# Kernel optimization log

Measured on AMD Instinct MI355X. Metric: run time of the kernel, lower is better.

## Reference

```python
import jax, jax.numpy as jnp
import numpy as np

N = 100000      # nodes
M_HE = 200000   # hyperedges
E = 2000000     # incidences (edge_index columns)
IN, HID, OUT, NT = 16, 64, 64, 2


def setup_inputs() -> dict:
    key = jax.random.key(0)
    ks = jax.random.split(key, 16)
    s = 0.05
    return {
        "x": jax.random.normal(ks[0], (N, IN), jnp.float32),
        "h_prev": jax.random.normal(ks[1], (N, HID), jnp.float32),
        "edge_nodes": jax.random.randint(ks[2], (E,), 0, N, dtype=jnp.int32),
        "edge_hedges": jax.random.randint(ks[3], (E,), 0, M_HE, dtype=jnp.int32),
        "edge_attr": jax.random.randint(ks[4], (E,), 0, NT, dtype=jnp.int32),
        "W_conv": jax.random.normal(ks[5], (NT, IN, HID), jnp.float32) * s,
        "b_conv": jax.random.normal(ks[6], (NT, HID), jnp.float32) * s,
        "W_mix": jax.random.normal(ks[7], (NT * HID, HID), jnp.float32) * s,
        "b_mix": jax.random.normal(ks[8], (HID,), jnp.float32) * s,
        "W_ih": jax.random.normal(ks[9], (3 * HID, HID), jnp.float32) * s,
        "W_hh": jax.random.normal(ks[10], (3 * HID, HID), jnp.float32) * s,
        "b_ih": jax.random.normal(ks[11], (3 * HID,), jnp.float32) * s,
        "b_hh": jax.random.normal(ks[12], (3 * HID,), jnp.float32) * s,
        "W_out": jax.random.normal(ks[13], (HID, OUT), jnp.float32) * s,
        "b_out": jax.random.normal(ks[14], (OUT,), jnp.float32) * s,
    }


def _hconv(x, W, b, nodes, hedges, mask_f):
    """PyG HypergraphConv: out = D^-1 H B^-1 H^T (x W) + b, restricted to
    incidences where mask_f==1 (replaces torch nonzero()-based slicing)."""
    xw = x @ W                                                   # [N, HID]
    Bdeg = jax.ops.segment_sum(mask_f, hedges, num_segments=M_HE)  # |e| per hyperedge
    Ddeg = jax.ops.segment_sum(mask_f, nodes, num_segments=N)      # deg per node
    Binv = jnp.where(Bdeg > 0, 1.0 / Bdeg, 0.0)
    Dinv = jnp.where(Ddeg > 0, 1.0 / Ddeg, 0.0)
    # node -> hyperedge gather/scatter
    e_feat = jax.ops.segment_sum(xw[nodes] * mask_f[:, None], hedges,
                                 num_segments=M_HE) * Binv[:, None]  # [M_HE, HID]
    # hyperedge -> node gather/scatter
    out = jax.ops.segment_sum(e_feat[hedges] * mask_f[:, None], nodes,
                              num_segments=N) * Dinv[:, None]        # [N, HID]
    return out + b


def reference(x, h_prev, edge_nodes, edge_hedges, edge_attr,
              W_conv, b_conv, W_mix, b_mix,
              W_ih, W_hh, b_ih, b_hh, W_out, b_out):
    outs = []
    for t in range(NT):  # fixed small loop over edge types
        mask_f = (edge_attr == t).astype(x.dtype)
        outs.append(_hconv(x, W_conv[t], b_conv[t], edge_nodes, edge_hedges, mask_f))
    h = jax.nn.relu(jnp.concatenate(outs, axis=1) @ W_mix + b_mix)  # [N, HID]
    # torch GRUCell(h, h_prev)
    gi = h @ W_ih.T + b_ih
    gh = h_prev @ W_hh.T + b_hh
    i_r, i_z, i_n = jnp.split(gi, 3, axis=1)
    h_r, h_z, h_n = jnp.split(gh, 3, axis=1)
    r = jax.nn.sigmoid(i_r + h_r)
    z = jax.nn.sigmoid(i_z + h_z)
    n = jnp.tanh(i_n + r * h_n)
    h_next = (1.0 - z) * n + z * h_prev
    pred_xyz = (h_next @ W_out + b_out)[:, :3]
    return h_next, pred_xyz
```

## Files before the change

kernel.cpp:

```cpp
#include <hip/hip_runtime.h>

#define NN      100000
#define MHE     200000
#define EE      2000000
#define H1      400000
#define K2N     200000
#define NB1     782
#define NB2     391
#define NCB2    320
#define CHK2    6250
#define FCN     375360
#define SCB2    367
#define CAP1    3584
#define CAP2    6144

typedef unsigned short u16;
typedef unsigned int   u32;
typedef unsigned long long ull;
typedef __attribute__((ext_vector_type(8))) short  s16x8;
typedef __attribute__((ext_vector_type(4))) float  f32x4;
typedef __attribute__((ext_vector_type(4))) unsigned int u32x4;

__device__ __forceinline__ float bf2f(u16 u) { return __uint_as_float(((u32)u) << 16); }
__device__ __forceinline__ u16 f2bf(float f) {
    u32 u = __float_as_uint(f);
    return (u16)((u + 0x7fffu + ((u >> 16) & 1u)) >> 16);
}
__device__ __forceinline__ float ldv(const void* p, long i, int isf32) {
    return isf32 ? ((const float*)p)[i] : bf2f(((const u16*)p)[i]);
}
__device__ __forceinline__ u16 ldb(const void* p, long i, int isf32) {
    return isf32 ? f2bf(((const float*)p)[i]) : ((const u16*)p)[i];
}
__device__ __forceinline__ void stv(void* p, long i, float v, int isf32) {
    if (isf32) ((float*)p)[i] = v;
    else       ((u16*)p)[i] = f2bf(v);
}

union FragU { s16x8 v; ull q[2]; u16 u[8]; };

__device__ __forceinline__ s16x8 ld8bf(const void* p, long off, int isf32) {
    FragU f;
    if (isf32) {
        const float* fp = (const float*)p + off;
        f32x4 a = *(const f32x4*)fp;
        f32x4 b = *(const f32x4*)(fp + 4);
        f.u[0]=f2bf(a[0]); f.u[1]=f2bf(a[1]); f.u[2]=f2bf(a[2]); f.u[3]=f2bf(a[3]);
        f.u[4]=f2bf(b[0]); f.u[5]=f2bf(b[1]); f.u[6]=f2bf(b[2]); f.u[7]=f2bf(b[3]);
    } else {
        u32x4 w = *(const u32x4*)((const u16*)p + off);
        f.q[0] = ((ull)w[1] << 32) | w[0];
        f.q[1] = ((ull)w[3] << 32) | w[2];
    }
    return f.v;
}

__device__ __forceinline__ float frcp_(float x) { return __builtin_amdgcn_rcpf(x); }
__device__ __forceinline__ float sigm(float x)  { return frcp_(1.f + __expf(-x)); }
__device__ __forceinline__ float tanhf_(float x){ return 1.f - 2.f * frcp_(1.f + __expf(2.f * x)); }

#define OFF_BKT1  0
#define OFF_BKT2  2000000
#define OFF_EXB   4000000
#define OFF_FSC   7200000
#define OFF_TOT   7575361
#define OFF_BCOMB 7575728
#define OFF_WIHB  7575792
#define OFF_WHHB  7581936
#define OFF_WCB   7588080
#define OFF_FLAG  7589104

__global__ void detect_kernel(const u32* __restrict__ xw, u32* __restrict__ flag) {
    __shared__ int cnt;
    if (threadIdx.x == 0) cnt = 0;
    __syncthreads();
    int hits = 0;
    for (int i = threadIdx.x; i < 1024; i += 256) {
        float v = bf2f((u16)(xw[i] & 0xffffu));
        if (!(fabsf(v) < 1e10f)) hits++;
    }
    atomicAdd(&cnt, hits);
    __syncthreads();
    if (threadIdx.x == 0) flag[0] = (cnt >= 16) ? 1u : 0u;
}

#define XBASE 26688
__global__ __launch_bounds__(256) void setup_kernel(
        const void* __restrict__ W_conv, const void* __restrict__ b_conv,
        const void* __restrict__ W_mix,  const void* __restrict__ b_mix,
        const void* __restrict__ W_ih,   const void* __restrict__ W_hh,
        float* __restrict__ bcomb, u16* __restrict__ Wihb, u16* __restrict__ Whhb,
        u16* __restrict__ Wcb, const u32* __restrict__ flag) {
    int isf = (int)flag[0];
    int gid = blockIdx.x * 256 + threadIdx.x;
    if (gid < 12288) {
        Wihb[gid] = ldb(W_ih, gid, isf);
    } else if (gid < 24576) {
        int i = gid - 12288;
        Whhb[i] = ldb(W_hh, i, isf);
    } else if (gid < 26624) {
        int i = gid - 24576;
        int j = i >> 5, k = i & 31;
        int t0 = k >> 4, kk = k & 15;
        float acc = 0.f;
        for (int c = 0; c < 64; c++)
            acc += ldv(W_conv, (t0 * 16 + kk) * 64 + c, isf) * ldv(W_mix, (t0 * 64 + c) * 64 + j, isf);
        Wcb[i] = f2bf(acc);
    } else if (gid < XBASE) {
        int j = gid - 26624;
        if (j < 64) {
            float acc = ldv(b_mix, j, isf);
            for (int c = 0; c < 128; c++)
                acc += ldv(b_conv, c, isf) * ldv(W_mix, c * 64 + j, isf);
            bcomb[j] = acc;
        }
    }
}

__global__ __launch_bounds__(1024) void countC(const int* __restrict__ en, const int* __restrict__ eh,
                                               const int* __restrict__ ea, int* __restrict__ fcnt) {
    __shared__ int c[NB1 + NB2];
    int g = blockIdx.x, tid = threadIdx.x;
    for (int i = tid; i < NB1 + NB2; i += 1024) c[i] = 0;
    __syncthreads();
    int s = g * CHK2;
    for (int i = s + tid; i < s + CHK2; i += 1024) {
        int t = ea[i];
        atomicAdd(&c[(t * MHE + eh[i]) >> 9], 1);
        atomicAdd(&c[NB1 + ((t * NN + en[i]) >> 9)], 1);
    }
    __syncthreads();
    for (int b = tid; b < NB1 + NB2; b += 1024) fcnt[b * NCB2 + g] = c[b];
}

__global__ __launch_bounds__(256) void scanA2(int* __restrict__ a, int* __restrict__ tot) {
    __shared__ int lds[256];
    int g = blockIdx.x, t = threadIdx.x;
    int base = g * 1024 + t * 4;
    int v[4]; int s = 0;
    #pragma unroll
    for (int j = 0; j < 4; j++) { v[j] = (base + j < FCN) ? a[base + j] : 0; s += v[j]; }
    lds[t] = s;
    __syncthreads();
    for (int d = 1; d < 256; d <<= 1) {
        int tmp = (t >= d) ? lds[t - d] : 0;
        __syncthreads();
        lds[t] += tmp;
        __syncthreads();
    }
    int run = lds[t] - s;
    #pragma unroll
    for (int j = 0; j < 4; j++) { if (base + j < FCN) a[base + j] = run; run += v[j]; }
    if (t == 255) tot[g] = lds[255];
}

__global__ __launch_bounds__(1024) void scanB2(int* __restrict__ tot) {
    __shared__ int lds[1024];
    int t = threadIdx.x;
    int v = (t < SCB2) ? tot[t] : 0;
    lds[t] = v;
    __syncthreads();
    for (int d = 1; d < 1024; d <<= 1) {
        int tmp = (t >= d) ? lds[t - d] : 0;
        __syncthreads();
        lds[t] += tmp;
        __syncthreads();
    }
    if (t < SCB2) tot[t] = lds[t] - v;
}

__global__ __launch_bounds__(256) void scanC2(int* __restrict__ a, const int* __restrict__ tot) {
    int g = blockIdx.x, t = threadIdx.x;
    int add = tot[g];
    int base = g * 1024 + t * 4;
    #pragma unroll
    for (int j = 0; j < 4; j++)
        if (base + j < FCN) a[base + j] += add;
    if (g == 0 && t == 0) a[FCN] = 2 * EE;
}

template<int SIDE>
__global__ __launch_bounds__(1024) void placeC(const int* __restrict__ en, const int* __restrict__ eh,
                                               const int* __restrict__ ea, const int* __restrict__ fscan,
                                               u32* __restrict__ bktout) {
    __shared__ u32 sarr[CHK2];
    __shared__ int sbuf[1024];
    __shared__ int cnt[NB1];
    __shared__ int loff[NB1];
    const int nb = SIDE ? NB2 : NB1;
    const int fbase = SIDE ? NB1 * NCB2 : 0;
    int g = blockIdx.x, tid = threadIdx.x;
    for (int b = tid; b < nb; b += 1024) {
        int idx = fbase + b * NCB2 + g;
        cnt[b] = fscan[idx + 1] - fscan[idx];
    }
    __syncthreads();
    int v = (tid < nb) ? cnt[tid] : 0;
    sbuf[tid] = v;
    __syncthreads();
    for (int d = 1; d < 1024; d <<= 1) {
        int tmp = (tid >= d) ? sbuf[tid - d] : 0;
        __syncthreads();
        sbuf[tid] += tmp;
        __syncthreads();
    }
    if (tid < nb) { loff[tid] = sbuf[tid] - v; cnt[tid] = 0; }
    __syncthreads();
    int s = g * CHK2;
    for (int i = s + tid; i < s + CHK2; i += 1024) {
        int t = ea[i]; int nd = en[i]; int hh = eh[i];
        int k = SIDE ? (t * NN + nd) : (t * MHE + hh);
        int b = k >> 9;
        int r = atomicAdd(&cnt[b], 1);
        u32 pay = SIDE ? (((u32)(k & 511) << 19) | (u32)(t * MHE + hh))
                       : (((u32)(k & 511) << 17) | (u32)nd);
        sarr[loff[b] + r] = pay;
    }
    __syncthreads();
    for (int s2 = tid; s2 < CHK2; s2 += 1024) {
        int lo = 0, hi = nb - 1;
        while (lo < hi) {
            int mid = (lo + hi + 1) >> 1;
            if (loff[mid] <= s2) lo = mid; else hi = mid - 1;
        }
        int gp = fscan[fbase + lo * NCB2 + g] + (s2 - loff[lo]);
        if (SIDE) gp -= EE;
        bktout[gp] = sarr[s2];
    }
}

__global__ __launch_bounds__(512) void hopA(const int* __restrict__ fscan, const u32* __restrict__ bkt1,
                                            const void* __restrict__ x, u32* __restrict__ exb,
                                            const u32* __restrict__ flag) {
    __shared__ int fcnt[512], foff[513], sbuf[512];
    __shared__ int snod[CAP1];
    int isf = (int)flag[0];
    int c = blockIdx.x, tid = threadIdx.x;
    int beg = fscan[c * NCB2], end = fscan[(c + 1) * NCB2];
    fcnt[tid] = 0;
    __syncthreads();
    for (int i = beg + tid; i < end; i += 512)
        atomicAdd(&fcnt[bkt1[i] >> 17], 1);
    __syncthreads();
    int v = fcnt[tid];
    sbuf[tid] = v;
    __syncthreads();
    for (int d = 1; d < 512; d <<= 1) {
        int tmp = (tid >= d) ? sbuf[tid - d] : 0;
        __syncthreads();
        sbuf[tid] += tmp;
        __syncthreads();
    }
    foff[tid] = sbuf[tid] - v;
    fcnt[tid] = 0;
    if (tid == 511) foff[512] = sbuf[511];
    __syncthreads();
    for (int i = beg + tid; i < end; i += 512) {
        u32 p = bkt1[i];
        int k = (int)(p >> 17);
        int r = atomicAdd(&fcnt[k], 1);
        snod[foff[k] + r] = (int)(p & 0x1FFFFu);
    }
    __syncthreads();
    int sub = tid & 7, grp = tid >> 3;
    for (int kk = grp; kk < 512; kk += 64) {
        int key = c * 512 + kk;
        if (key >= H1) break;
        int fb = foff[kk], fe = foff[kk + 1];
        float a0 = 0.f, a1 = 0.f;
        if (isf) {
            const float* xf = (const float*)x;
            for (int j = fb; j < fe; j++) {
                long n0 = (long)snod[j];
                a0 += xf[n0 * 16 + 2 * sub];
                a1 += xf[n0 * 16 + 2 * sub + 1];
            }
        } else {
            const u32* xu = (const u32*)x;
            for (int j = fb; j < fe; j++) {
                u32 w = xu[(long)snod[j] * 8 + sub];
                a0 += bf2f((u16)(w & 0xffffu));
                a1 += bf2f((u16)(w >> 16));
            }
        }
        int d = fe - fb;
        float inv = d > 0 ? 1.0f / (float)d : 0.f;
        exb[(long)key * 8 + sub] = (u32)f2bf(a0 * inv) | ((u32)f2bf(a1 * inv) << 16);
    }
}

__global__ __launch_bounds__(512) void hopB(const int* __restrict__ fscan, const u32* __restrict__ bkt2,
                                            const u32* __restrict__ exb, u32* __restrict__ aggb) {
    __shared__ int fcnt[512], foff[513], sbuf[512];
    __shared__ int shed[CAP2];
    int c = blockIdx.x, tid = threadIdx.x;
    int beg = fscan[NB1 * NCB2 + c * NCB2] - EE;
    int end = fscan[NB1 * NCB2 + (c + 1) * NCB2] - EE;
    fcnt[tid] = 0;
    __syncthreads();
    for (int i = beg + tid; i < end; i += 512)
        atomicAdd(&fcnt[bkt2[i] >> 19], 1);
    __syncthreads();
    int v = fcnt[tid];
    sbuf[tid] = v;
    __syncthreads();
    for (int d = 1; d < 512; d <<= 1) {
        int tmp = (tid >= d) ? sbuf[tid - d] : 0;
        __syncthreads();
        sbuf[tid] += tmp;
        __syncthreads();
    }
    foff[tid] = sbuf[tid] - v;
    fcnt[tid] = 0;
    if (tid == 511) foff[512] = sbuf[511];
    __syncthreads();
    for (int i = beg + tid; i < end; i += 512) {
        u32 p = bkt2[i];
        int k = (int)(p >> 19);
        int r = atomicAdd(&fcnt[k], 1);
        shed[foff[k] + r] = (int)(p & 0x7FFFFu);
    }
    __syncthreads();
    int sub = tid & 7, grp = tid >> 3;
    for (int kk = grp; kk < 512; kk += 64) {
        int key = c * 512 + kk;
        if (key >= K2N) break;
        int fb = foff[kk], fe = foff[kk + 1];
        float a0 = 0.f, a1 = 0.f;
        for (int j = fb; j < fe; j++) {
            u32 w = exb[(long)shed[j] * 8 + sub];
            a0 += bf2f((u16)(w & 0xffffu));
            a1 += bf2f((u16)(w >> 16));
        }
        int d = fe - fb;
        float inv = d > 0 ? 1.0f / (float)d : 0.f;
        aggb[(long)key * 8 + sub] = (u32)f2bf(a0 * inv) | ((u32)f2bf(a1 * inv) << 16);
    }
}

__global__ __launch_bounds__(256) void epilogue(const u32* __restrict__ aggb,
                                                const float* __restrict__ bcomb,
                                                const u16* __restrict__ Wihb,
                                                const u16* __restrict__ Whhb,
                                                const u16* __restrict__ Wcb,
                                                const void* __restrict__ b_ih, const void* __restrict__ b_hh,
                                                const void* __restrict__ h_prev,
                                                const void* __restrict__ W_out, const void* __restrict__ b_out,
                                                void* __restrict__ out,
                                                const u32* __restrict__ flag) {
    __shared__ u16 hA[4][16][72];
    __shared__ float cb[8][64];
    __shared__ float cbo[3];
    int isf = (int)flag[0];
    int tid = threadIdx.x;
    if (tid < 64) {
        int j = tid;
        cb[0][j] = bcomb[j];
        cb[1][j] = ldv(b_ih, j, isf)       + ldv(b_hh, j, isf);
        cb[2][j] = ldv(b_ih, 64 + j, isf)  + ldv(b_hh, 64 + j, isf);
        cb[3][j] = ldv(b_ih, 128 + j, isf);
        cb[4][j] = ldv(b_hh, 128 + j, isf);
        cb[5][j] = ldv(W_out, (long)j * 64 + 0, isf);
        cb[6][j] = ldv(W_out, (long)j * 64 + 1, isf);
        cb[7][j] = ldv(W_out, (long)j * 64 + 2, isf);
        if (j < 3) cbo[j] = ldv(b_out, j, isf);
    }
    __syncthreads();
    int w = tid >> 6, lane = tid & 63;
    int cl = lane & 15, q = lane >> 4;
    u16* hAw = &hA[w][0][0];

    for (int wt = blockIdx.x * 4 + w; wt < NN / 16; wt += gridDim.x * 4) {
        long nb = (long)wt * 16;
        {
            int t0 = q >> 1;
            long nidx = nb + cl;
            const u32* ap = aggb + ((long)t0 * NN + nidx) * 8 + (q & 1) * 4;
            u32x4 aw = *(const u32x4*)ap;
            FragU fa;
            fa.q[0] = ((ull)aw[1] << 32) | aw[0];
            fa.q[1] = ((ull)aw[3] << 32) | aw[2];
            #pragma unroll
            for (int c = 0; c < 4; c++) {
                f32x4 hacc = (f32x4){0.f, 0.f, 0.f, 0.f};
                s16x8 bfr = *(const s16x8*)(Wcb + (c * 16 + cl) * 32 + q * 8);
                hacc = __builtin_amdgcn_mfma_f32_16x16x32_bf16(fa.v, bfr, hacc, 0, 0, 0);
                float bc = cb[0][c * 16 + cl];
                #pragma unroll
                for (int reg = 0; reg < 4; reg++) {
                    float hv = fmaxf(hacc[reg] + bc, 0.f);
                    hAw[(q * 4 + reg) * 72 + c * 16 + cl] = f2bf(hv);
                }
            }
        }
        asm volatile("" ::: "memory");
        const u16* hrow = hAw + cl * 72;
        FragU ha0, ha1;
        #pragma unroll
        for (int j = 0; j < 8; j++) {
            ha0.u[j] = hrow[q * 8 + j];
            ha1.u[j] = hrow[32 + q * 8 + j];
        }
        s16x8 hp0 = ld8bf(h_prev, (nb + cl) * 64 + q * 8, isf);
        s16x8 hp1 = ld8bf(h_prev, (nb + cl) * 64 + 32 + q * 8, isf);

        float p0[4] = {0,0,0,0}, p1[4] = {0,0,0,0}, p2[4] = {0,0,0,0};
        #pragma unroll
        for (int ch = 0; ch < 2; ch++) {
            f32x4 accr[2], accz[2], accin[2], acchn[2];
            #pragma unroll
            for (int cc = 0; cc < 2; cc++) {
                int j = (ch * 2 + cc) * 16 + cl;
                float br_ = cb[1][j], bz_ = cb[2][j], bi_ = cb[3][j], bh_ = cb[4][j];
                accr[cc]  = (f32x4){br_, br_, br_, br_};
                accz[cc]  = (f32x4){bz_, bz_, bz_, bz_};
                accin[cc] = (f32x4){bi_, bi_, bi_, bi_};
                acchn[cc] = (f32x4){bh_, bh_, bh_, bh_};
            }
            #pragma unroll
            for (int s = 0; s < 2; s++) {
                s16x8 hf  = s ? ha1.v : ha0.v;
                s16x8 hpf = s ? hp1 : hp0;
                int ko = s * 32 + q * 8;
                #pragma unroll
                for (int cc = 0; cc < 2; cc++) {
                    int rr = (ch * 2 + cc) * 16 + cl;
                    {
                        s16x8 bir = *(const s16x8*)(Wihb + (long)rr * 64 + ko);
                        accr[cc]  = __builtin_amdgcn_mfma_f32_16x16x32_bf16(hf,  bir,  accr[cc], 0, 0, 0);
                    }
                    {
                        s16x8 bhr = *(const s16x8*)(Whhb + (long)rr * 64 + ko);
                        accr[cc]  = __builtin_amdgcn_mfma_f32_16x16x32_bf16(hpf, bhr,  accr[cc], 0, 0, 0);
                    }
                    {
                        s16x8 biz = *(const s16x8*)(Wihb + (long)(64 + rr) * 64 + ko);
                        accz[cc]  = __builtin_amdgcn_mfma_f32_16x16x32_bf16(hf,  biz,  accz[cc], 0, 0, 0);
                    }
                    {
                        s16x8 bhz = *(const s16x8*)(Whhb + (long)(64 + rr) * 64 + ko);
                        accz[cc]  = __builtin_amdgcn_mfma_f32_16x16x32_bf16(hpf, bhz,  accz[cc], 0, 0, 0);
                    }
                    {
                        s16x8 bin2 = *(const s16x8*)(Wihb + (long)(128 + rr) * 64 + ko);
                        accin[cc] = __builtin_amdgcn_mfma_f32_16x16x32_bf16(hf,  bin2, accin[cc], 0, 0, 0);
                    }
                    {
                        s16x8 bhn2 = *(const s16x8*)(Whhb + (long)(128 + rr) * 64 + ko);
                        acchn[cc] = __builtin_amdgcn_mfma_f32_16x16x32_bf16(hpf, bhn2, acchn[cc], 0, 0, 0);
                    }
                }
            }
            #pragma unroll
            for (int cc = 0; cc < 2; cc++) {
                int j = (ch * 2 + cc) * 16 + cl;
                float wo0 = cb[5][j], wo1 = cb[6][j], wo2 = cb[7][j];
                #pragma unroll
                for (int reg = 0; reg < 4; reg++) {
                    float rr = sigm(accr[cc][reg]);
                    float zz = sigm(accz[cc][reg]);
                    float ng = tanhf_(accin[cc][reg] + rr * acchn[cc][reg]);
                    long n = nb + q * 4 + reg;
                    float hp = ldv(h_prev, n * 64 + j, isf);
                    float hx = (1.f - zz) * ng + zz * hp;
                    stv(out, n * 64 + j, hx, isf);
                    p0[reg] += hx * wo0;
                    p1[reg] += hx * wo1;
                    p2[reg] += hx * wo2;
                }
            }
        }
        #pragma unroll
        for (int reg = 0; reg < 4; reg++) {
            #pragma unroll
            for (int off2 = 1; off2 < 16; off2 <<= 1) {
                p0[reg] += __shfl_xor(p0[reg], off2);
                p1[reg] += __shfl_xor(p1[reg], off2);
                p2[reg] += __shfl_xor(p2[reg], off2);
            }
        }
        if (cl == 0) {
            #pragma unroll
            for (int reg = 0; reg < 4; reg++) {
                long n = nb + q * 4 + reg;
                long pb = (long)NN * 64 + n * 3;
                stv(out, pb + 0, p0[reg] + cbo[0], isf);
                stv(out, pb + 1, p1[reg] + cbo[1], isf);
                stv(out, pb + 2, p2[reg] + cbo[2], isf);
            }
        }
    }
}

extern "C" void kernel_launch(void* const* d_in, const int* in_sizes, int n_in,
                              void* d_out, int out_size, void* d_ws, size_t ws_size,
                              hipStream_t stream) {
    const void* x      = d_in[0];
    const void* h_prev = d_in[1];
    const int* en      = (const int*)d_in[2];
    const int* eh      = (const int*)d_in[3];
    const int* ea      = (const int*)d_in[4];
    const void* W_conv = d_in[5];
    const void* b_conv = d_in[6];
    const void* W_mix  = d_in[7];
    const void* b_mix  = d_in[8];
    const void* W_ih   = d_in[9];
    const void* W_hh   = d_in[10];
    const void* b_ih   = d_in[11];
    const void* b_hh   = d_in[12];
    const void* W_out  = d_in[13];
    const void* b_out  = d_in[14];
    void* out          = d_out;

    float* ws    = (float*)d_ws;
    u32* bkt1    = (u32*)(ws + OFF_BKT1);
    u32* bkt2    = (u32*)(ws + OFF_BKT2);
    u32* exb     = (u32*)(ws + OFF_EXB);
    int* fscan   = (int*)(ws + OFF_FSC);
    u32* aggb    = (u32*)(ws + OFF_BKT1);
    float* bcomb = ws + OFF_BCOMB;
    u16* Wihb    = (u16*)(ws + OFF_WIHB);
    u16* Whhb    = (u16*)(ws + OFF_WHHB);
    u16* Wcb     = (u16*)(ws + OFF_WCB);
    u32* flag    = (u32*)(ws + OFF_FLAG);
    int* tot     = (int*)(ws + OFF_TOT);

    detect_kernel<<<1, 256, 0, stream>>>((const u32*)x, flag);
    setup_kernel<<<(XBASE + 255) / 256, 256, 0, stream>>>(
        W_conv, b_conv, W_mix, b_mix, W_ih, W_hh,
        bcomb, Wihb, Whhb, Wcb, flag);
    countC<<<NCB2, 1024, 0, stream>>>(en, eh, ea, fscan);
    scanA2<<<SCB2, 256, 0, stream>>>(fscan, tot);
    scanB2<<<1, 1024, 0, stream>>>(tot);
    scanC2<<<SCB2, 256, 0, stream>>>(fscan, tot);
    placeC<0><<<NCB2, 1024, 0, stream>>>(en, eh, ea, fscan, bkt1);
    placeC<1><<<NCB2, 1024, 0, stream>>>(en, eh, ea, fscan, bkt2);
    hopA<<<NB1, 512, 0, stream>>>(fscan, bkt1, x, exb, flag);
    hopB<<<NB2, 512, 0, stream>>>(fscan, bkt2, exb, aggb);
    epilogue<<<1563, 256, 0, stream>>>(aggb, bcomb, Wihb, Whhb, Wcb,
                                       b_ih, b_hh, h_prev, W_out, b_out, out, flag);
}
```

Baseline: 353.7 us.

## Stage GRU weights in swizzled LDS and prefetch next tile in epilogue

The epilogue now copies the combined W_ih/W_hh bf16 weights (48 KB) into shared memory with an XOR swizzle, and reads MFMA B fragments from there instead of from global memory. It software-pipelines the per-tile aggb and h_prev loads one iteration ahead and cuts the grid from 1563 to 512 blocks so each block amortizes the staging cost over more tiles. This assumes Wihb and Whhb are laid out contiguously in the workspace. The larger LDS use lowers occupancy, and the fewer blocks reduce parallelism.

```diff
diff --git a/kernel.cpp b/kernel.cpp
--- a/kernel.cpp
+++ b/kernel.cpp
@@ -13,6 +13,7 @@
 #define SCB2    367
 #define CAP1    3584
 #define CAP2    6144
+#define NT      6250
 
 typedef unsigned short u16;
 typedef unsigned int   u32;
@@ -340,19 +341,30 @@
 
 __global__ __launch_bounds__(256) void epilogue(const u32* __restrict__ aggb,
                                                 const float* __restrict__ bcomb,
-                                                const u16* __restrict__ Wihb,
-                                                const u16* __restrict__ Whhb,
+                                                const u16* __restrict__ WihbG,
                                                 const u16* __restrict__ Wcb,
                                                 const void* __restrict__ b_ih, const void* __restrict__ b_hh,
                                                 const void* __restrict__ h_prev,
                                                 const void* __restrict__ W_out, const void* __restrict__ b_out,
                                                 void* __restrict__ out,
                                                 const u32* __restrict__ flag) {
+    __shared__ u16 Wl[24576];
     __shared__ u16 hA[4][16][72];
     __shared__ float cb[8][64];
     __shared__ float cbo[3];
     int isf = (int)flag[0];
     int tid = threadIdx.x;
+    {
+        const u32* gw = (const u32*)WihbG;
+        for (int i = tid; i < 12288; i += 256) {
+            u32 v = gw[i];
+            int row = i >> 5;
+            int wb = (i & 31) * 4;
+            int slot = wb >> 4, rem = wb & 15;
+            int wb2 = (((slot ^ (row & 7)) << 4) | rem);
+            *(u32*)(Wl + ((row << 6) + (wb2 >> 1))) = v;
+        }
+    }
     if (tid < 64) {
         int j = tid;
         cb[0][j] = bcomb[j];
@@ -369,17 +381,33 @@
     int w = tid >> 6, lane = tid & 63;
     int cl = lane & 15, q = lane >> 4;
     u16* hAw = &hA[w][0][0];
-
-    for (int wt = blockIdx.x * 4 + w; wt < NN / 16; wt += gridDim.x * 4) {
+    int t0 = q >> 1;
+
+    int wt = blockIdx.x * 4 + w;
+    const int WSTRIDE = gridDim.x * 4;
+
+    u32x4 aw; s16x8 hpA, hpB;
+    if (wt < NT) {
         long nb = (long)wt * 16;
+        aw  = *(const u32x4*)(aggb + ((long)t0 * NN + nb + cl) * 8 + (q & 1) * 4);
+        hpA = ld8bf(h_prev, (nb + cl) * 64 + q * 8, isf);
+        hpB = ld8bf(h_prev, (nb + cl) * 64 + 32 + q * 8, isf);
+    }
+    while (wt < NT) {
+        int cwt = wt;
+        u32x4 caw = aw; s16x8 chp0 = hpA, chp1 = hpB;
+        wt += WSTRIDE;
+        if (wt < NT) {
+            long nb = (long)wt * 16;
+            aw  = *(const u32x4*)(aggb + ((long)t0 * NN + nb + cl) * 8 + (q & 1) * 4);
+            hpA = ld8bf(h_prev, (nb + cl) * 64 + q * 8, isf);
+            hpB = ld8bf(h_prev, (nb + cl) * 64 + 32 + q * 8, isf);
+        }
+        long nb = (long)cwt * 16;
         {
-            int t0 = q >> 1;
-            long nidx = nb + cl;
-            const u32* ap = aggb + ((long)t0 * NN + nidx) * 8 + (q & 1) * 4;
-            u32x4 aw = *(const u32x4*)ap;
             FragU fa;
-            fa.q[0] = ((ull)aw[1] << 32) | aw[0];
-            fa.q[1] = ((ull)aw[3] << 32) | aw[2];
+            fa.q[0] = ((ull)caw[1] << 32) | caw[0];
+            fa.q[1] = ((ull)caw[3] << 32) | caw[2];
             #pragma unroll
             for (int c = 0; c < 4; c++) {
                 f32x4 hacc = (f32x4){0.f, 0.f, 0.f, 0.f};
@@ -401,8 +429,6 @@
             ha0.u[j] = hrow[q * 8 + j];
             ha1.u[j] = hrow[32 + q * 8 + j];
         }
-        s16x8 hp0 = ld8bf(h_prev, (nb + cl) * 64 + q * 8, isf);
-        s16x8 hp1 = ld8bf(h_prev, (nb + cl) * 64 + 32 + q * 8, isf);
 
         float p0[4] = {0,0,0,0}, p1[4] = {0,0,0,0}, p2[4] = {0,0,0,0};
         #pragma unroll
@@ -420,35 +446,24 @@
             #pragma unroll
             for (int s = 0; s < 2; s++) {
                 s16x8 hf  = s ? ha1.v : ha0.v;
-                s16x8 hpf = s ? hp1 : hp0;
-                int ko = s * 32 + q * 8;
+                s16x8 hpf = s ? chp1 : chp0;
+                int sl8 = ((s * 4 + q) ^ (cl & 7)) * 8;
                 #pragma unroll
                 for (int cc = 0; cc < 2; cc++) {
                     int rr = (ch * 2 + cc) * 16 + cl;
-                    {
-                        s16x8 bir = *(const s16x8*)(Wihb + (long)rr * 64 + ko);
-                        accr[cc]  = __builtin_amdgcn_mfma_f32_16x16x32_bf16(hf,  bir,  accr[cc], 0, 0, 0);
-                    }
-                    {
-                        s16x8 bhr = *(const s16x8*)(Whhb + (long)rr * 64 + ko);
-                        accr[cc]  = __builtin_amdgcn_mfma_f32_16x16x32_bf16(hpf, bhr,  accr[cc], 0, 0, 0);
-                    }
-                    {
-                        s16x8 biz = *(const s16x8*)(Wihb + (long)(64 + rr) * 64 + ko);
-                        accz[cc]  = __builtin_amdgcn_mfma_f32_16x16x32_bf16(hf,  biz,  accz[cc], 0, 0, 0);
-                    }
-                    {
-                        s16x8 bhz = *(const s16x8*)(Whhb + (long)(64 + rr) * 64 + ko);
-                        accz[cc]  = __builtin_amdgcn_mfma_f32_16x16x32_bf16(hpf, bhz,  accz[cc], 0, 0, 0);
-                    }
-                    {
-                        s16x8 bin2 = *(const s16x8*)(Wihb + (long)(128 + rr) * 64 + ko);
-                        accin[cc] = __builtin_amdgcn_mfma_f32_16x16x32_bf16(hf,  bin2, accin[cc], 0, 0, 0);
-                    }
-                    {
-                        s16x8 bhn2 = *(const s16x8*)(Whhb + (long)(128 + rr) * 64 + ko);
-                        acchn[cc] = __builtin_amdgcn_mfma_f32_16x16x32_bf16(hpf, bhn2, acchn[cc], 0, 0, 0);
-                    }
+                    const u16* pw = Wl + rr * 64 + sl8;
+                    s16x8 bir  = *(const s16x8*)(pw);
+                    s16x8 biz  = *(const s16x8*)(pw + 4096);
+                    s16x8 bin2 = *(const s16x8*)(pw + 8192);
+                    s16x8 bhr  = *(const s16x8*)(pw + 12288);
+                    s16x8 bhz  = *(const s16x8*)(pw + 16384);
+                    s16x8 bhn2 = *(const s16x8*)(pw + 20480);
+                    accr[cc]  = __builtin_amdgcn_mfma_f32_16x16x32_bf16(hf,  bir,  accr[cc], 0, 0, 0);
+                    accr[cc]  = __builtin_amdgcn_mfma_f32_16x16x32_bf16(hpf, bhr,  accr[cc], 0, 0, 0);
+                    accz[cc]  = __builtin_amdgcn_mfma_f32_16x16x32_bf16(hf,  biz,  accz[cc], 0, 0, 0);
+                    accz[cc]  = __builtin_amdgcn_mfma_f32_16x16x32_bf16(hpf, bhz,  accz[cc], 0, 0, 0);
+                    accin[cc] = __builtin_amdgcn_mfma_f32_16x16x32_bf16(hf,  bin2, accin[cc], 0, 0, 0);
+                    acchn[cc] = __builtin_amdgcn_mfma_f32_16x16x32_bf16(hpf, bhn2, acchn[cc], 0, 0, 0);
                 }
             }
             #pragma unroll
@@ -537,6 +552,6 @@
     placeC<1><<<NCB2, 1024, 0, stream>>>(en, eh, ea, fscan, bkt2);
     hopA<<<NB1, 512, 0, stream>>>(fscan, bkt1, x, exb, flag);
     hopB<<<NB2, 512, 0, stream>>>(fscan, bkt2, exb, aggb);
-    epilogue<<<1563, 256, 0, stream>>>(aggb, bcomb, Wihb, Whhb, Wcb,
-                                       b_ih, b_hh, h_prev, W_out, b_out, out, flag);
-}
+    epilogue<<<512, 256, 0, stream>>>(aggb, bcomb, Wihb, Wcb,
+                                      b_ih, b_hh, h_prev, W_out, b_out, out, flag);
+}
```

After: 312.2 us. 1.13x faster.
